# Kernel tuning notes

Hardware: AMD Instinct MI355X
Metric: run time of the kernel (lower is better)

## Reference

```python
import jax, jax.numpy as jnp
import numpy as np

NUM_HEADS = 16
ROPE_THETA = 10000.0


def _rope_tables(S, d_k):
    # angles[s, j] = s / theta^(2j/d_k), j over d_k/2 pairs
    inv_freq = 1.0 / (ROPE_THETA ** (jnp.arange(0, d_k, 2, dtype=jnp.float32) / d_k))
    angles = jnp.arange(S, dtype=jnp.float32)[:, None] * inv_freq[None, :]  # [S, d_k/2]
    # repeat_interleave(…, 2, dim=-1) -> [S, d_k]
    cos2 = jnp.repeat(jnp.cos(angles), 2, axis=-1)
    sin2 = jnp.repeat(jnp.sin(angles), 2, axis=-1)
    return cos2, sin2


def _rotate_half(x):
    x_even = x[..., 0::2]
    x_odd = x[..., 1::2]
    return jnp.stack([-x_odd, x_even], axis=-1).reshape(x.shape)


def _apply_rope(x, cos2, sin2):
    # x: [B, H, S, d_k]; cos2/sin2: [S, d_k] broadcast over B, H
    return x * cos2 + _rotate_half(x) * sin2


def setup_inputs() -> dict:
    key = jax.random.key(0)
    k1, k2, k3, k4, k5 = jax.random.split(key, 5)
    B, S, D = 2, 2048, 1024
    std = (2.0 / (D + D)) ** 0.5
    x = jax.random.normal(k1, (B, S, D), dtype=jnp.float32)
    Wq = jax.random.normal(k2, (D, D), dtype=jnp.float32) * std
    Wk = jax.random.normal(k3, (D, D), dtype=jnp.float32) * std
    Wv = jax.random.normal(k4, (D, D), dtype=jnp.float32) * std
    Wo = jax.random.normal(k5, (D, D), dtype=jnp.float32) * std
    return {"x": x, "Wq": Wq, "Wk": Wk, "Wv": Wv, "Wo": Wo}


def reference(x, Wq, Wk, Wv, Wo):
    B, S, D = x.shape
    H = NUM_HEADS
    d_k = D // H
    # Linear is y = W x with W[d_out, d_in]
    Q = jnp.einsum('bsd,ed->bse', x, Wq).reshape(B, S, H, d_k).transpose(0, 2, 1, 3)
    K = jnp.einsum('bsd,ed->bse', x, Wk).reshape(B, S, H, d_k).transpose(0, 2, 1, 3)
    V = jnp.einsum('bsd,ed->bse', x, Wv).reshape(B, S, H, d_k).transpose(0, 2, 1, 3)
    cos2, sin2 = _rope_tables(S, d_k)
    Q = _apply_rope(Q, cos2, sin2)
    K = _apply_rope(K, cos2, sin2)
    scores = jnp.einsum('bhqd,bhkd->bhqk', Q, K) / jnp.sqrt(jnp.float32(d_k))
    causal = jnp.tril(jnp.ones((S, S), dtype=bool))
    scores = jnp.where(causal, scores, -jnp.inf)
    attn = jax.nn.softmax(scores, axis=-1)
    out = jnp.einsum('bhqk,bhkd->bhqd', attn, V)  # [B,H,S,d_k]
    out = out.transpose(0, 2, 1, 3).reshape(B, S, D)
    return jnp.einsum('bsd,ed->bse', out, Wo)
```

## Files before the change

### kernel.cpp

```cpp
#include <hip/hip_runtime.h>
#include <hip/hip_bf16.h>

typedef float f32x4 __attribute__((ext_vector_type(4)));
typedef __bf16 bf16x8 __attribute__((ext_vector_type(8)));

static constexpr int S  = 2048;
static constexpr int D  = 1024;
static constexpr int DK = 64;
static constexpr int KDIM = 1024;
static constexpr float QSCALE = 0.18033688f;

#define AS1 __attribute__((address_space(1)))
#define AS3 __attribute__((address_space(3)))

__device__ __forceinline__ void glds16(const void* g, void* l) {
  __builtin_amdgcn_global_load_lds((const AS1 void*)g, (AS3 void*)l, 16, 0, 0);
}

__device__ __forceinline__ unsigned cvtpk(float lo, float hi) {
  unsigned r;
  asm("v_cvt_pk_bf16_f32 %0, %1, %2" : "=v"(r) : "v"(lo), "v"(hi));
  return r;
}

__device__ __forceinline__ void pl32swap(unsigned& a, unsigned& b) {
  asm("v_permlane32_swap_b32 %0, %1" : "+v"(a), "+v"(b));
}

__device__ __forceinline__ float fexp2(float x) {
  float r;
  asm("v_exp_f32 %0, %1" : "=v"(r) : "v"(x));
  return r;
}

__device__ __forceinline__ int kperm64(int k) {
  const int kf = k >> 4, hs = (k >> 2) & 3, r = k & 3;
  const bool inl = ((kf & 1) == (hs >> 1));
  const int h = inl ? hs : (hs ^ 2);
  const int j = inl ? r : (r + 4);
  return ((kf >> 1) << 5) + (h << 3) + j;
}

__global__ __launch_bounds__(256) void pre_kernel(
    const float* __restrict__ x,  const float* __restrict__ Wq,
    const float* __restrict__ Wk, const float* __restrict__ Wv,
    const float* __restrict__ Wo,
    __hip_bfloat16* __restrict__ xb, __hip_bfloat16* __restrict__ Wcat,
    __hip_bfloat16* __restrict__ Wob,
    float* __restrict__ cosT, float* __restrict__ sinT) {
  const int gid = blockIdx.x * 256 + threadIdx.x;
  if (gid < 2097152) {
    const float* src;
    __hip_bfloat16* dst;
    int off;
    if (gid < 1048576)      { src = x;  dst = xb;             off = gid; }
    else if (gid < 1310720) { src = Wq; dst = Wcat;           off = gid - 1048576; }
    else if (gid < 1572864) { src = Wk; dst = Wcat + 1048576; off = gid - 1310720; }
    else if (gid < 1835008) { src = Wv; dst = Wcat + 2097152; off = gid - 1572864; }
    else                    { src = Wo; dst = Wob;            off = gid - 1835008; }
    float4 v = reinterpret_cast<const float4*>(src)[off];
    union { ushort4 u; __hip_bfloat16 h[4]; } o;
    o.h[0] = __float2bfloat16(v.x);
    o.h[1] = __float2bfloat16(v.y);
    o.h[2] = __float2bfloat16(v.z);
    o.h[3] = __float2bfloat16(v.w);
    reinterpret_cast<ushort4*>(dst)[off] = o.u;
  } else {
    const int idx = gid - 2097152;
    const int s = idx >> 5, fi = idx & 31;
    float invf = powf(10000.0f, -(float)(2 * fi) / 64.0f);
    float ang = (float)s * invf;
    cosT[idx] = cosf(ang);
    sinT[idx] = sinf(ang);
  }
}

template <int MODE>
__global__ __launch_bounds__(256) void gemm_nt_kernel(
    const __hip_bfloat16* __restrict__ A,
    const __hip_bfloat16* __restrict__ Bw,
    float* __restrict__ Cf,
    __hip_bfloat16* __restrict__ Qr,
    __hip_bfloat16* __restrict__ Kr,
    __hip_bfloat16* __restrict__ Vt,
    const float* __restrict__ cosT,
    const float* __restrict__ sinT,
    int Ncols) {
  __shared__ __attribute__((aligned(16))) __hip_bfloat16 Asm[128 * 32];
  __shared__ __attribute__((aligned(16))) __hip_bfloat16 Bsm[128 * 32];
  const int tid = threadIdx.x;
  const int nbn = Ncols >> 7;
  const int cpx = gridDim.x >> 3;
  const int swz = (blockIdx.x & 7) * cpx + (blockIdx.x >> 3);
  const int bm = swz / nbn;
  const int bn = swz % nbn;
  const int m0 = bm << 7, n0 = bn << 7;
  const int lane = tid & 63;
  const int wid = tid >> 6;
  const int wm = wid >> 1, wn = wid & 1;
  const int r16 = lane & 15, hf = lane >> 4;

  f32x4 acc[4][4];
#pragma unroll
  for (int i = 0; i < 4; ++i)
#pragma unroll
    for (int j = 0; j < 4; ++j) acc[i][j] = (f32x4)0.0f;

  for (int k0 = 0; k0 < KDIM; k0 += 32) {
    __syncthreads();
#pragma unroll
    for (int i = 0; i < 2; ++i) {
      const int idx = i * 256 + tid;
      const int row = idx >> 2;
      const int cb = (idx & 3) << 4;
      glds16((const char*)A + ((size_t)(m0 + row) * KDIM + k0) * 2 + cb,
             (char*)Asm + idx * 16);
      glds16((const char*)Bw + ((size_t)(n0 + row) * KDIM + k0) * 2 + cb,
             (char*)Bsm + idx * 16);
    }
    __syncthreads();
    bf16x8 af[4], bfr[4];
#pragma unroll
    for (int mi = 0; mi < 4; ++mi)
      af[mi] = *(const bf16x8*)((const char*)Asm +
                                ((wm << 6) + (mi << 4) + r16) * 64 + hf * 16);
#pragma unroll
    for (int ni = 0; ni < 4; ++ni)
      bfr[ni] = *(const bf16x8*)((const char*)Bsm +
                                 ((wn << 6) + (ni << 4) + r16) * 64 + hf * 16);
#pragma unroll
    for (int mi = 0; mi < 4; ++mi)
#pragma unroll
      for (int ni = 0; ni < 4; ++ni)
        acc[mi][ni] = __builtin_amdgcn_mfma_f32_16x16x32_bf16(af[mi], bfr[ni],
                                                              acc[mi][ni], 0, 0, 0);
  }

  if constexpr (MODE == 0) {
#pragma unroll
    for (int mi = 0; mi < 4; ++mi) {
      const int rowb = m0 + (wm << 6) + (mi << 4) + (hf << 2);
#pragma unroll
      for (int ni = 0; ni < 4; ++ni) {
        const int col = n0 + (wn << 6) + (ni << 4) + r16;
#pragma unroll
        for (int r = 0; r < 4; ++r)
          Cf[(size_t)(rowb + r) * Ncols + col] = acc[mi][ni][r];
      }
    }
  } else {
    const int proj = n0 >> 10;
#pragma unroll
    for (int mi = 0; mi < 4; ++mi) {
      const int rowb = m0 + (wm << 6) + (mi << 4) + (hf << 2);
      const int b = rowb >> 11;
      const int sbase = rowb & 2047;
#pragma unroll
      for (int ni = 0; ni < 4; ++ni) {
        const int col = n0 + (wn << 6) + (ni << 4) + r16;
        const int ecol = col & 1023;
        const int h = ecol >> 6, dk = ecol & 63;
        if (proj < 2) {
#pragma unroll
          for (int r = 0; r < 4; ++r) {
            float v = acc[mi][ni][r];
            const int s = sbase + r;
            float p = __shfl_xor(v, 1, 64);
            const int fi = dk >> 1;
            const float c = cosT[(s << 5) + fi];
            const float sn = sinT[(s << 5) + fi];
            float ov = v * c + ((dk & 1) ? p : -p) * sn;
            if (proj == 0) ov *= QSCALE;
            __hip_bfloat16* dst = (proj == 0) ? Qr : Kr;
            dst[((size_t)((b << 4) + h) * S + s) * DK + dk] = __float2bfloat16(ov);
          }
        } else {
          const int sp0 = (sbase & ~63) | kperm64(sbase & 63);
          union { ushort4 u; __hip_bfloat16 hh[4]; } vp;
#pragma unroll
          for (int r = 0; r < 4; ++r)
            vp.hh[r] = __float2bfloat16(acc[mi][ni][r]);
          *reinterpret_cast<ushort4*>(
              &Vt[((size_t)((b << 4) + h) * DK + dk) * S + sp0]) = vp.u;
        }
      }
    }
  }
}

__global__ __launch_bounds__(256) void attn_kernel(
    const __hip_bfloat16* __restrict__ Q,
    const __hip_bfloat16* __restrict__ Kr,
    const __hip_bfloat16* __restrict__ Vp,
    __hip_bfloat16* __restrict__ AO,
    __hip_bfloat16* __restrict__ Opart,
    float* __restrict__ ml) {
  __shared__ __attribute__((aligned(16))) __hip_bfloat16 Ks[2][64 * 64];
  __shared__ __attribute__((aligned(16))) __hip_bfloat16 Vs[2][64 * 64];
  static const int T[8][3] = {{0, 1, 23},  {2, 5, 20},  {3, 9, 17}, {4, 15, 14},
                              {6, 16, 21}, {7, 11, 18}, {10, 8, 22}, {12, 13, 19}};
  const int tid = threadIdx.x;
  const int lane = tid & 63, wid = tid >> 6;
  const int r16 = lane & 15, hf = lane >> 4;
  const bool hi32 = (lane >= 32);
  const int bh = blockIdx.x & 31;
  const int cg = (blockIdx.x >> 5) & 7;
  const int slot = blockIdx.x >> 8;
  const int item = T[cg][slot];
  const int g = item / 3, j = item - 3 * g;
  int qt, k0, k1;
  bool dosplit;
  if (j < 2) {
    qt = 15 - g;
    const int nt = (qt << 1) + 2;
    k0 = j ? (nt >> 1) : 0;
    k1 = j ? nt : (nt >> 1);
    dosplit = true;
  } else {
    qt = 7 - g;
    k0 = 0;
    k1 = (qt << 1) + 2;
    dosplit = false;
  }
  const __hip_bfloat16* Qh = Q + (size_t)bh * S * DK;
  const __hip_bfloat16* Kh = Kr + (size_t)bh * S * DK;
  const __hip_bfloat16* Vh = Vp + (size_t)bh * DK * S;

  const int qbase = (qt << 7) + (wid << 5);

  bf16x8 bq[2][2];
#pragma unroll
  for (int qf = 0; qf < 2; ++qf)
#pragma unroll
    for (int ks = 0; ks < 2; ++ks)
      bq[qf][ks] = *(const bf16x8*)(Qh + (size_t)(qbase + (qf << 4) + r16) * DK +
                                    ks * 32 + hf * 8);

  f32x4 o[2][4];
#pragma unroll
  for (int qf = 0; qf < 2; ++qf)
#pragma unroll
    for (int f = 0; f < 4; ++f) o[qf][f] = (f32x4)0.0f;
  float m[2] = {-1e30f, -1e30f}, l[2] = {0.0f, 0.0f};

#define STAGE(bufi, t)                                                         \
  {                                                                            \
    _Pragma("unroll") for (int i = 0; i < 2; ++i) {                            \
      const int idx = i * 256 + tid;                                           \
      const int row = idx >> 3;                                                \
      const int cb = (idx & 7) << 4;                                           \
      const int scb = cb ^ ((row & 7) << 4);                                   \
      glds16((const char*)Kh + ((size_t)(((t) << 6) + row) * DK) * 2 + scb,    \
             (char*)(&Ks[bufi][0]) + idx * 16);                                \
      glds16((const char*)Vh + ((size_t)row * S + ((t) << 6)) * 2 + scb,       \
             (char*)(&Vs[bufi][0]) + idx * 16);                                \
    }                                                                          \
  }

  STAGE(0, k0);
  __syncthreads();

  for (int kt = k0; kt < k1; ++kt) {
    const int cur = (kt - k0) & 1;
    if (kt + 1 < k1) STAGE(cur ^ 1, kt + 1);

    f32x4 p[2][4];
#pragma unroll
    for (int qf = 0; qf < 2; ++qf)
#pragma unroll
      for (int kf = 0; kf < 4; ++kf) p[qf][kf] = (f32x4)0.0f;
    __builtin_amdgcn_s_setprio(1);
#pragma unroll
    for (int ks = 0; ks < 2; ++ks) {
#pragma unroll
      for (int kf = 0; kf < 4; ++kf) {
        const int krow = (kf << 4) + r16;
        const int cb = (ks << 6) + (hf << 4);
        const bf16x8 ak = *(const bf16x8*)((const char*)(&Ks[cur][0]) +
                                           krow * 128 + (cb ^ ((krow & 7) << 4)));
#pragma unroll
        for (int qf = 0; qf < 2; ++qf)
          p[qf][kf] = __builtin_amdgcn_mfma_f32_16x16x32_bf16(ak, bq[qf][ks],
                                                              p[qf][kf], 0, 0, 0);
      }
    }
    __builtin_amdgcn_s_setprio(0);

    if (kt >= (qt << 1)) {
#pragma unroll
      for (int qf = 0; qf < 2; ++qf) {
        const int qg = qbase + (qf << 4) + r16;
#pragma unroll
        for (int kf = 0; kf < 4; ++kf)
#pragma unroll
          for (int r = 0; r < 4; ++r) {
            const int kg = (kt << 6) + (kf << 4) + (hf << 2) + r;
            if (kg > qg) p[qf][kf][r] = -1e30f;
          }
      }
    }

#pragma unroll
    for (int qf = 0; qf < 2; ++qf) {
      f32x4 m4;
#pragma unroll
      for (int e = 0; e < 4; ++e)
        m4[e] = fmaxf(fmaxf(p[qf][0][e], p[qf][1][e]),
                      fmaxf(p[qf][2][e], p[qf][3][e]));
      float t = fmaxf(fmaxf(m4[0], m4[1]), fmaxf(m4[2], m4[3]));
      t = fmaxf(t, __shfl_xor(t, 16, 64));
      t = fmaxf(t, __shfl_xor(t, 32, 64));
      if (t > m[qf] + 8.0f) {
        const float scl = fexp2(m[qf] - t);
        m[qf] = t;
        l[qf] *= scl;
#pragma unroll
        for (int f = 0; f < 4; ++f)
#pragma unroll
          for (int r = 0; r < 4; ++r) o[qf][f][r] *= scl;
      }
      float ss = 0.0f;
#pragma unroll
      for (int kf = 0; kf < 4; ++kf)
#pragma unroll
        for (int r = 0; r < 4; ++r) {
          const float e = fexp2(p[qf][kf][r] - m[qf]);
          p[qf][kf][r] = e;
          ss += e;
        }
      ss += __shfl_xor(ss, 16, 64);
      ss += __shfl_xor(ss, 32, 64);
      l[qf] += ss;
    }

    union PW { unsigned u[4]; bf16x8 v; };
    PW pb[2][2];
#pragma unroll
    for (int qf = 0; qf < 2; ++qf) {
      unsigned w[4][2];
#pragma unroll
      for (int kf = 0; kf < 4; ++kf) {
        w[kf][0] = cvtpk(p[qf][kf][0], p[qf][kf][1]);
        w[kf][1] = cvtpk(p[qf][kf][2], p[qf][kf][3]);
      }
#pragma unroll
      for (int ks = 0; ks < 2; ++ks) {
        unsigned a0 = w[2 * ks][0], b0 = w[2 * ks + 1][0];
        unsigned a1 = w[2 * ks][1], b1 = w[2 * ks + 1][1];
        pb[qf][ks].u[0] = hi32 ? b0 : a0;
        pb[qf][ks].u[1] = hi32 ? b1 : a1;
        pl32swap(a0, b0);
        pl32swap(a1, b1);
        pb[qf][ks].u[2] = hi32 ? a0 : b0;
        pb[qf][ks].u[3] = hi32 ? a1 : b1;
      }
    }

    __builtin_amdgcn_s_setprio(1);
#pragma unroll
    for (int ks = 0; ks < 2; ++ks) {
#pragma unroll
      for (int f = 0; f < 4; ++f) {
        const int vrow = (f << 4) + r16;
        const int cb = (ks << 6) + (hf << 4);
        const bf16x8 av = *(const bf16x8*)((const char*)(&Vs[cur][0]) +
                                           vrow * 128 + (cb ^ ((vrow & 7) << 4)));
#pragma unroll
        for (int qf = 0; qf < 2; ++qf)
          o[qf][f] = __builtin_amdgcn_mfma_f32_16x16x32_bf16(av, pb[qf][ks].v,
                                                             o[qf][f], 0, 0, 0);
      }
    }
    __builtin_amdgcn_s_setprio(0);

    __syncthreads();
  }
#undef STAGE

  if (!dosplit) {
    const int b = bh >> 4, h = bh & 15;
#pragma unroll
    for (int qf = 0; qf < 2; ++qf) {
      const float inv = 1.0f / l[qf];
      const int q = qbase + (qf << 4) + r16;
#pragma unroll
      for (int f = 0; f < 4; ++f)
#pragma unroll
        for (int r = 0; r < 4; ++r) {
          const int dv = (f << 4) + (hf << 2) + r;
          AO[((size_t)b * S + q) * D + (h << 6) + dv] =
              __float2bfloat16(o[qf][f][r] * inv);
        }
    }
  } else {
    const int sidx = (g << 1) | j;
    __hip_bfloat16* op = Opart + (((size_t)bh * 16 + sidx) << 13);
    float* mlp = ml + (((size_t)bh * 16 + sidx) << 8);
#pragma unroll
    for (int qf = 0; qf < 2; ++qf) {
      const float inv = 1.0f / l[qf];
      const int rowin = (wid << 5) + (qf << 4) + r16;
#pragma unroll
      for (int f = 0; f < 4; ++f)
#pragma unroll
        for (int r = 0; r < 4; ++r) {
          const int dv = (f << 4) + (hf << 2) + r;
          op[rowin * 64 + dv] = __float2bfloat16(o[qf][f][r] * inv);
        }
      if (hf == 0) {
        mlp[rowin * 2] = m[qf];
        mlp[rowin * 2 + 1] = l[qf];
      }
    }
  }
}

__global__ __launch_bounds__(256) void merge_kernel(
    const __hip_bfloat16* __restrict__ Opart,
    const float* __restrict__ ml,
    __hip_bfloat16* __restrict__ AO) {
  const int rg = blockIdx.x * 256 + threadIdx.x;
  const int bh = rg >> 10;
  const int rem = rg & 1023;
  const int gq = rem >> 7;
  const int rowin = rem & 127;
  const int s0 = bh * 16 + (gq << 1), s1 = s0 + 1;
  const float m0 = ml[(s0 << 8) + rowin * 2], l0 = ml[(s0 << 8) + rowin * 2 + 1];
  const float m1 = ml[(s1 << 8) + rowin * 2], l1 = ml[(s1 << 8) + rowin * 2 + 1];
  const float mx = fmaxf(m0, m1);
  float w0 = l0 * fexp2(m0 - mx), w1 = l1 * fexp2(m1 - mx);
  const float inv = 1.0f / (w0 + w1);
  w0 *= inv;
  w1 *= inv;
  const bf16x8* p0 = (const bf16x8*)(Opart + (((size_t)s0) << 13) + rowin * 64);
  const bf16x8* p1 = (const bf16x8*)(Opart + (((size_t)s1) << 13) + rowin * 64);
  const int b = bh >> 4, h = bh & 15;
  const int q = ((15 - gq) << 7) + rowin;
  bf16x8* dst = (bf16x8*)(AO + ((size_t)b * S + q) * D + (h << 6));
#pragma unroll
  for (int i = 0; i < 8; ++i) {
    bf16x8 a = p0[i], c = p1[i];
    bf16x8 r;
#pragma unroll
    for (int e = 0; e < 8; ++e)
      r[e] = (__bf16)(w0 * (float)a[e] + w1 * (float)c[e]);
    dst[i] = r;
  }
}

extern "C" void kernel_launch(void* const* d_in, const int* in_sizes, int n_in,
                              void* d_out, int out_size, void* d_ws, size_t ws_size,
                              hipStream_t stream) {
  (void)in_sizes; (void)n_in; (void)out_size; (void)ws_size;
  const float* x  = (const float*)d_in[0];
  const float* Wq = (const float*)d_in[1];
  const float* Wk = (const float*)d_in[2];
  const float* Wv = (const float*)d_in[3];
  const float* Wo = (const float*)d_in[4];
  float* out = (float*)d_out;
  char* ws = (char*)d_ws;
  const size_t MB = (size_t)1 << 20;
  __hip_bfloat16* xb   = (__hip_bfloat16*)(ws);
  __hip_bfloat16* Wcat = (__hip_bfloat16*)(ws + 8 * MB);
  __hip_bfloat16* Wob  = (__hip_bfloat16*)(ws + 14 * MB);
  __hip_bfloat16* Qr   = (__hip_bfloat16*)(ws + 16 * MB);
  __hip_bfloat16* Kr   = (__hip_bfloat16*)(ws + 24 * MB);
  __hip_bfloat16* Vt   = (__hip_bfloat16*)(ws + 32 * MB);
  __hip_bfloat16* AO   = (__hip_bfloat16*)(ws + 40 * MB);
  float* cosT = (float*)(ws + 48 * MB);
  float* sinT = (float*)(ws + 48 * MB + 256 * 1024);
  __hip_bfloat16* Opart = (__hip_bfloat16*)(ws);
  float* mlbuf = (float*)(ws + 8 * MB);

  pre_kernel<<<8448, 256, 0, stream>>>(x, Wq, Wk, Wv, Wo, xb, Wcat, Wob,
                                       cosT, sinT);
  gemm_nt_kernel<1><<<(4096 / 128) * (3072 / 128), 256, 0, stream>>>(
      xb, Wcat, nullptr, Qr, Kr, Vt, cosT, sinT, 3072);
  attn_kernel<<<32 * 24, 256, 0, stream>>>(Qr, Kr, Vt, AO, Opart, mlbuf);
  merge_kernel<<<128, 256, 0, stream>>>(Opart, mlbuf, AO);
  gemm_nt_kernel<0><<<(4096 / 128) * (1024 / 128), 256, 0, stream>>>(
      AO, Wob, out, nullptr, nullptr, nullptr, nullptr, nullptr, 1024);
}
```

Before: 217.9 us.

## Double-buffer GEMM LDS staging, change smem layout, use 64x128 tiles for output projection

Templates the GEMM on tile shape and adds a two-stage LDS ping-pong, so the global-to-LDS loads for the next K step are issued before the MFMAs on the current one, and one barrier per iteration is removed. The LDS layout changes from row-major to chunk-major (16-byte column chunk outer, row inner), which alters the bank pattern of the fragment reads. The output projection now uses 64x128 tiles, doubling its block count to improve CU occupancy on the small GEMM. The trade-off is double the LDS per block, which can lower residency. There is also a possible race: the next-stage load is issued right after the previous iteration's trailing barrier, with no wait on the asynchronous LDS writes before the following compute.

```diff
diff --git a/kernel.cpp b/kernel.cpp
--- a/kernel.cpp
+++ b/kernel.cpp
@@ -75,7 +75,7 @@
   }
 }
 
-template <int MODE>
+template <int MODE, int BM, int BN>
 __global__ __launch_bounds__(256) void gemm_nt_kernel(
     const __hip_bfloat16* __restrict__ A,
     const __hip_bfloat16* __restrict__ Bw,
@@ -86,63 +86,80 @@
     const float* __restrict__ cosT,
     const float* __restrict__ sinT,
     int Ncols) {
-  __shared__ __attribute__((aligned(16))) __hip_bfloat16 Asm[128 * 32];
-  __shared__ __attribute__((aligned(16))) __hip_bfloat16 Bsm[128 * 32];
+  constexpr int ACH = BM * 4;
+  constexpr int BCH = BN * 4;
+  constexpr int TCH = ACH + BCH;
+  constexpr int NI = (BM == 128) ? 4 : 2;
+  __shared__ __attribute__((aligned(16))) char smem[2][TCH * 16];
   const int tid = threadIdx.x;
-  const int nbn = Ncols >> 7;
+  const int nbn = Ncols / BN;
   const int cpx = gridDim.x >> 3;
   const int swz = (blockIdx.x & 7) * cpx + (blockIdx.x >> 3);
   const int bm = swz / nbn;
   const int bn = swz % nbn;
-  const int m0 = bm << 7, n0 = bn << 7;
+  const int m0 = bm * BM, n0 = bn * BN;
   const int lane = tid & 63;
   const int wid = tid >> 6;
-  const int wm = wid >> 1, wn = wid & 1;
   const int r16 = lane & 15, hf = lane >> 4;
-
-  f32x4 acc[4][4];
+  const int wmoff = (BM == 128) ? ((wid >> 1) << 6) : 0;
+  const int wnoff = (BM == 128) ? ((wid & 1) << 6) : (wid << 5);
+
+  f32x4 acc[4][NI];
 #pragma unroll
   for (int i = 0; i < 4; ++i)
 #pragma unroll
-    for (int j = 0; j < 4; ++j) acc[i][j] = (f32x4)0.0f;
-
-  for (int k0 = 0; k0 < KDIM; k0 += 32) {
-    __syncthreads();
-#pragma unroll
-    for (int i = 0; i < 2; ++i) {
+    for (int j = 0; j < NI; ++j) acc[i][j] = (f32x4)0.0f;
+
+  auto stage = [&](int bufi, int k0) {
+#pragma unroll
+    for (int i = 0; i < TCH / 256; ++i) {
       const int idx = i * 256 + tid;
-      const int row = idx >> 2;
-      const int cb = (idx & 3) << 4;
-      glds16((const char*)A + ((size_t)(m0 + row) * KDIM + k0) * 2 + cb,
-             (char*)Asm + idx * 16);
-      glds16((const char*)Bw + ((size_t)(n0 + row) * KDIM + k0) * 2 + cb,
-             (char*)Bsm + idx * 16);
-    }
-    __syncthreads();
-    bf16x8 af[4], bfr[4];
+      char* dst = &smem[bufi][idx * 16];
+      if (idx < ACH) {
+        const int row = idx % BM, c = idx / BM;
+        glds16((const char*)A + ((size_t)(m0 + row) * KDIM + k0) * 2 + c * 16,
+               dst);
+      } else {
+        const int bi = idx - ACH;
+        const int row = bi % BN, c = bi / BN;
+        glds16((const char*)Bw + ((size_t)(n0 + row) * KDIM + k0) * 2 + c * 16,
+               dst);
+      }
+    }
+  };
+
+  stage(0, 0);
+  __syncthreads();
+
+  for (int kb = 0; kb < KDIM / 32; ++kb) {
+    const int cur = kb & 1;
+    if (kb + 1 < KDIM / 32) stage(cur ^ 1, (kb + 1) * 32);
+
+    const char* Ab = smem[cur];
+    const char* Bb = smem[cur] + ACH * 16;
+    bf16x8 af[4], bfr[NI];
 #pragma unroll
     for (int mi = 0; mi < 4; ++mi)
-      af[mi] = *(const bf16x8*)((const char*)Asm +
-                                ((wm << 6) + (mi << 4) + r16) * 64 + hf * 16);
-#pragma unroll
-    for (int ni = 0; ni < 4; ++ni)
-      bfr[ni] = *(const bf16x8*)((const char*)Bsm +
-                                 ((wn << 6) + (ni << 4) + r16) * 64 + hf * 16);
+      af[mi] = *(const bf16x8*)(Ab + (hf * BM + wmoff + mi * 16 + r16) * 16);
+#pragma unroll
+    for (int ni = 0; ni < NI; ++ni)
+      bfr[ni] = *(const bf16x8*)(Bb + (hf * BN + wnoff + ni * 16 + r16) * 16);
 #pragma unroll
     for (int mi = 0; mi < 4; ++mi)
 #pragma unroll
-      for (int ni = 0; ni < 4; ++ni)
+      for (int ni = 0; ni < NI; ++ni)
         acc[mi][ni] = __builtin_amdgcn_mfma_f32_16x16x32_bf16(af[mi], bfr[ni],
                                                               acc[mi][ni], 0, 0, 0);
+    __syncthreads();
   }
 
   if constexpr (MODE == 0) {
 #pragma unroll
     for (int mi = 0; mi < 4; ++mi) {
-      const int rowb = m0 + (wm << 6) + (mi << 4) + (hf << 2);
-#pragma unroll
-      for (int ni = 0; ni < 4; ++ni) {
-        const int col = n0 + (wn << 6) + (ni << 4) + r16;
+      const int rowb = m0 + wmoff + (mi << 4) + (hf << 2);
+#pragma unroll
+      for (int ni = 0; ni < NI; ++ni) {
+        const int col = n0 + wnoff + (ni << 4) + r16;
 #pragma unroll
         for (int r = 0; r < 4; ++r)
           Cf[(size_t)(rowb + r) * Ncols + col] = acc[mi][ni][r];
@@ -152,12 +169,12 @@
     const int proj = n0 >> 10;
 #pragma unroll
     for (int mi = 0; mi < 4; ++mi) {
-      const int rowb = m0 + (wm << 6) + (mi << 4) + (hf << 2);
+      const int rowb = m0 + wmoff + (mi << 4) + (hf << 2);
       const int b = rowb >> 11;
       const int sbase = rowb & 2047;
 #pragma unroll
-      for (int ni = 0; ni < 4; ++ni) {
-        const int col = n0 + (wn << 6) + (ni << 4) + r16;
+      for (int ni = 0; ni < NI; ++ni) {
+        const int col = n0 + wnoff + (ni << 4) + r16;
         const int ecol = col & 1023;
         const int h = ecol >> 6, dk = ecol & 63;
         if (proj < 2) {
@@ -474,10 +491,10 @@
 
   pre_kernel<<<8448, 256, 0, stream>>>(x, Wq, Wk, Wv, Wo, xb, Wcat, Wob,
                                        cosT, sinT);
-  gemm_nt_kernel<1><<<(4096 / 128) * (3072 / 128), 256, 0, stream>>>(
+  gemm_nt_kernel<1, 128, 128><<<(4096 / 128) * (3072 / 128), 256, 0, stream>>>(
       xb, Wcat, nullptr, Qr, Kr, Vt, cosT, sinT, 3072);
   attn_kernel<<<32 * 24, 256, 0, stream>>>(Qr, Kr, Vt, AO, Opart, mlbuf);
   merge_kernel<<<128, 256, 0, stream>>>(Opart, mlbuf, AO);
-  gemm_nt_kernel<0><<<(4096 / 128) * (1024 / 128), 256, 0, stream>>>(
+  gemm_nt_kernel<0, 64, 128><<<(4096 / 64) * (1024 / 128), 256, 0, stream>>>(
       AO, Wob, out, nullptr, nullptr, nullptr, nullptr, nullptr, 1024);
 }
```

After: 226.8 us. 1.04x slower.
